# Optimization experiments

Hardware: AMD Instinct MI355X
Metric: run time of the kernel (lower is better)

## Reference

```python
import jax, jax.numpy as jnp
import numpy as np

N_NODES = 40000
N_EDGES = 640000
D = 128
BN_EPS = 1e-5
GATE_EPS = 1e-6


def _linear_params(key, d_in, d_out):
    kw, kb = jax.random.split(key)
    bound = 1.0 / np.sqrt(d_in)
    W = jax.random.uniform(kw, (d_out, d_in), jnp.float32, -bound, bound)
    b = jax.random.uniform(kb, (d_out,), jnp.float32, -bound, bound)
    return W, b


def setup_inputs() -> dict:
    key = jax.random.key(0)
    ks = jax.random.split(key, 8)
    x = jax.random.normal(ks[0], (N_NODES, D), jnp.float32)
    edge_index = jax.random.randint(ks[1], (2, N_EDGES), 0, N_NODES, jnp.int64)
    edge_attr = jax.random.normal(ks[2], (N_EDGES, D), jnp.float32)
    W_src_gate, b_src_gate = _linear_params(ks[3], D, D)
    W_dst_gate, b_dst_gate = _linear_params(ks[4], D, D)
    W_edge_gate, b_edge_gate = _linear_params(ks[5], D, D)
    W_src_update, b_src_update = _linear_params(ks[6], D, D)
    W_dst_update, b_dst_update = _linear_params(ks[7], D, D)
    return dict(
        x=x, edge_index=edge_index, edge_attr=edge_attr,
        W_src_gate=W_src_gate, b_src_gate=b_src_gate,
        W_dst_gate=W_dst_gate, b_dst_gate=b_dst_gate,
        W_edge_gate=W_edge_gate, b_edge_gate=b_edge_gate,
        W_src_update=W_src_update, b_src_update=b_src_update,
        W_dst_update=W_dst_update, b_dst_update=b_dst_update,
        bn_nodes_gamma=jnp.ones((D,), jnp.float32), bn_nodes_beta=jnp.zeros((D,), jnp.float32),
        bn_edges_gamma=jnp.ones((D,), jnp.float32), bn_edges_beta=jnp.zeros((D,), jnp.float32),
    )


def _batch_norm(z, gamma, beta):
    # training-mode BN: batch mean, biased variance (torch semantics)
    mean = jnp.mean(z, axis=0)
    var = jnp.mean(jnp.square(z - mean), axis=0)
    return gamma * (z - mean) * jax.lax.rsqrt(var + BN_EPS) + beta


def reference(x, edge_index, edge_attr,
              W_src_gate, b_src_gate, W_dst_gate, b_dst_gate,
              W_edge_gate, b_edge_gate, W_src_update, b_src_update,
              W_dst_update, b_dst_update,
              bn_nodes_gamma, bn_nodes_beta, bn_edges_gamma, bn_edges_beta):
    row, col = edge_index[0], edge_index[1]
    num_nodes = x.shape[0]
    x_row = x[row]                      # [E, D] gather
    x_col = x[col]                      # [E, D] gather
    e_src = x_row @ W_src_gate.T + b_src_gate
    e_dst = x_col @ W_dst_gate.T + b_dst_gate
    m = e_src + e_dst + edge_attr @ W_edge_gate.T + b_edge_gate  # [E, D]
    sigma = jax.nn.sigmoid(m)
    h_weighted = (x_col @ W_dst_update.T + b_dst_update) * sigma
    h_sum = jax.ops.segment_sum(h_weighted, col, num_segments=num_nodes)
    sigma_sum = jax.ops.segment_sum(sigma, col, num_segments=num_nodes)
    h_normalized = h_sum / (sigma_sum + GATE_EPS)
    x_new = x @ W_src_update.T + b_src_update + h_normalized
    x_new = jax.nn.softplus(_batch_norm(x_new, bn_nodes_gamma, bn_nodes_beta))
    y_new = jax.nn.softplus(_batch_norm(m, bn_edges_gamma, bn_edges_beta))
    x_new = x + x_new          # residual
    y_new = edge_attr + y_new  # residual
    return (x_new, y_new)
```

## Files before the change

kernel.cpp:

```cpp
#include <hip/hip_runtime.h>

#define NN 40000
#define NE 640000

typedef unsigned short u16;
typedef unsigned int u32;
typedef __attribute__((ext_vector_type(4))) float f32x4;
typedef __attribute__((ext_vector_type(8))) __bf16 bf16x8;

#define LSTR 132
#define TPW 8

__device__ __forceinline__ float bf2f(u16 u) { return __uint_as_float(((u32)u) << 16); }
__device__ __forceinline__ u16 f2bf(float f) {
  u32 u = __float_as_uint(f);
  u32 r = 0x7fffu + ((u >> 16) & 1u);
  return (u16)((u + r) >> 16);
}
__device__ __forceinline__ float splus(float v) {
  return fmaxf(v, 0.0f) + __logf(1.0f + __expf(-fabsf(v)));
}

__global__ void sniff_k(const u32* __restrict__ gamma, const u32* __restrict__ eidx,
                        u32* __restrict__ flags) {
  if (threadIdx.x == 0) {
    flags[0] = (gamma[0] == 0x3F803F80u) ? 1u : 0u;
    u32 odd = eidx[1] | eidx[3] | eidx[5] | eidx[7] |
              eidx[9] | eidx[11] | eidx[13] | eidx[15];
    flags[1] = (odd == 0u) ? 1u : 0u;
  }
}

__device__ __forceinline__ int load_col(const void* eidx, int e, u32 i64) {
  int nc = i64 ? (int)((const u32*)eidx)[2 * ((size_t)NE + e)]
               : ((const int*)eidx)[NE + e];
  return min(max(nc, 0), NN - 1);
}
__device__ __forceinline__ int load_row(const void* eidx, int e, u32 i64) {
  int nr = i64 ? (int)((const u32*)eidx)[2 * (size_t)e]
               : ((const int*)eidx)[e];
  return min(max(nr, 0), NN - 1);
}

__global__ __launch_bounds__(256) void wconv5_k(
    const float* __restrict__ W0, const float* __restrict__ W1,
    const float* __restrict__ W2, const float* __restrict__ W3,
    const float* __restrict__ W4, u16* __restrict__ out) {
  int i = blockIdx.x * 256 + threadIdx.x;
  int mtx = blockIdx.y;
  const float* W = (mtx == 0) ? W0 : (mtx == 1) ? W1 : (mtx == 2) ? W2
                 : (mtx == 3) ? W3 : W4;
  out[mtx * 16384 + i] = f2bf(W[i]);
}

__device__ __forceinline__ bf16x8 a_frag(const float* __restrict__ row, int kbase) {
  float4 f0 = *(const float4*)(row + kbase);
  float4 f1 = *(const float4*)(row + kbase + 4);
  bf16x8 a;
  a[0] = (__bf16)f0.x; a[1] = (__bf16)f0.y; a[2] = (__bf16)f0.z; a[3] = (__bf16)f0.w;
  a[4] = (__bf16)f1.x; a[5] = (__bf16)f1.y; a[6] = (__bf16)f1.z; a[7] = (__bf16)f1.w;
  return a;
}

__device__ __forceinline__ bf16x8 cvt8(float4 a, float4 b) {
  bf16x8 r;
  r[0] = (__bf16)a.x; r[1] = (__bf16)a.y; r[2] = (__bf16)a.z; r[3] = (__bf16)a.w;
  r[4] = (__bf16)b.x; r[5] = (__bf16)b.y; r[6] = (__bf16)b.z; r[7] = (__bf16)b.w;
  return r;
}

__device__ __forceinline__ void gemm16(const bf16x8 af[4], const u16* __restrict__ Wb,
                                       const float* __restrict__ bias, int lane,
                                       f32x4 acc[8]) {
  int l15 = lane & 15, lk = lane >> 4;
#pragma unroll
  for (int n = 0; n < 8; ++n) {
    float bv = bias[n * 16 + l15];
    acc[n] = (f32x4){bv, bv, bv, bv};
  }
#pragma unroll
  for (int n = 0; n < 8; ++n) {
    const u16* bp = Wb + (size_t)(n * 16 + l15) * 128 + lk * 8;
#pragma unroll
    for (int k = 0; k < 4; ++k) {
      bf16x8 b = *(const bf16x8*)(bp + 32 * k);
      acc[n] = __builtin_amdgcn_mfma_f32_16x16x32_bf16(af[k], b, acc[n], 0, 0, 0);
    }
  }
}

__device__ __forceinline__ void store_tile(u16* __restrict__ out, int m0, int lane,
                                           const f32x4 acc[8]) {
  int l15 = lane & 15, lk = lane >> 4;
#pragma unroll
  for (int n = 0; n < 8; ++n)
#pragma unroll
    for (int r = 0; r < 4; ++r)
      out[(size_t)(m0 + lk * 4 + r) * 128 + n * 16 + l15] = f2bf(acc[n][r]);
}

__global__ __launch_bounds__(256) void node_gemm_k(
    const float* __restrict__ x, const u16* __restrict__ Wb,
    const float* __restrict__ B0, const float* __restrict__ B1,
    const float* __restrict__ B2, const float* __restrict__ B3,
    u16* __restrict__ o0, u16* __restrict__ o1,
    u16* __restrict__ o2, u16* __restrict__ o3) {
  int tid = threadIdx.x, lane = tid & 63, w = tid >> 6;
  int m0 = blockIdx.x * 64 + w * 16;
  int l15 = lane & 15, lk = lane >> 4;
  const float* arow = x + (size_t)(m0 + l15) * 128;
  bf16x8 af[4];
#pragma unroll
  for (int k = 0; k < 4; ++k) af[k] = a_frag(arow, 32 * k + 8 * lk);
  f32x4 acc[8];
  gemm16(af, Wb + 0 * 16384, B0, lane, acc); store_tile(o0, m0, lane, acc);
  gemm16(af, Wb + 1 * 16384, B1, lane, acc); store_tile(o1, m0, lane, acc);
  gemm16(af, Wb + 2 * 16384, B2, lane, acc); store_tile(o2, m0, lane, acc);
  gemm16(af, Wb + 3 * 16384, B3, lane, acc); store_tile(o3, m0, lane, acc);
}

__global__ __launch_bounds__(256, 2) void edge_gemm_k(
    const float* __restrict__ ea, const u16* __restrict__ Wgb,
    const float* __restrict__ Bg, u16* __restrict__ mge) {
  __shared__ u16 mt[4][16][LSTR];
  int tid = threadIdx.x, lane = tid & 63, w = tid >> 6;
  int l15 = lane & 15, lk = lane >> 4;

  bf16x8 bf[8][4];
#pragma unroll
  for (int n = 0; n < 8; ++n)
#pragma unroll
    for (int k = 0; k < 4; ++k)
      bf[n][k] = *(const bf16x8*)(Wgb + (size_t)(n * 16 + l15) * 128 + lk * 8 + 32 * k);
  float bias[8];
#pragma unroll
  for (int n = 0; n < 8; ++n) bias[n] = Bg[n * 16 + l15];

  int base = (blockIdx.x * 4 + w) * (TPW * 16);
  const float* aptr = ea + (size_t)(base + l15) * 128 + 8 * lk;

  float4 tmp[8];
#pragma unroll
  for (int k = 0; k < 4; ++k) {
    tmp[2 * k]     = *(const float4*)(aptr + 32 * k);
    tmp[2 * k + 1] = *(const float4*)(aptr + 32 * k + 4);
  }
  bf16x8 af[4];
#pragma unroll
  for (int k = 0; k < 4; ++k) af[k] = cvt8(tmp[2 * k], tmp[2 * k + 1]);

  for (int t = 0; t < TPW; ++t) {
    if (t + 1 < TPW) {
      const float* anx = aptr + (size_t)(t + 1) * 16 * 128;
#pragma unroll
      for (int k = 0; k < 4; ++k) {
        tmp[2 * k]     = *(const float4*)(anx + 32 * k);
        tmp[2 * k + 1] = *(const float4*)(anx + 32 * k + 4);
      }
    }
    f32x4 acc[8];
#pragma unroll
    for (int n = 0; n < 8; ++n)
      acc[n] = (f32x4){bias[n], bias[n], bias[n], bias[n]};
#pragma unroll
    for (int n = 0; n < 8; ++n)
#pragma unroll
      for (int k = 0; k < 4; ++k)
        acc[n] = __builtin_amdgcn_mfma_f32_16x16x32_bf16(af[k], bf[n][k], acc[n], 0, 0, 0);
    if (t + 1 < TPW) {
#pragma unroll
      for (int k = 0; k < 4; ++k) af[k] = cvt8(tmp[2 * k], tmp[2 * k + 1]);
    }
    int e0 = base + t * 16;
#pragma unroll
    for (int n = 0; n < 8; ++n)
#pragma unroll
      for (int r = 0; r < 4; ++r)
        mt[w][lk * 4 + r][n * 16 + l15] = f2bf(acc[n][r]);
#pragma unroll
    for (int it = 0; it < 4; ++it) {
      int row = lane >> 2, ch = (lane & 3) + 4 * it;
      uint4 v = *(const uint4*)&mt[w][row][ch * 8];
      *(uint4*)(mge + (size_t)(e0 + row) * 128 + ch * 8) = v;
    }
  }
}

__global__ __launch_bounds__(256) void hist_k(const void* __restrict__ eidx,
                                              u32* __restrict__ cnt,
                                              const u32* __restrict__ flags) {
  int e = blockIdx.x * 256 + threadIdx.x;
  atomicAdd(&cnt[load_col(eidx, e, flags[1])], 1u);
}

__global__ __launch_bounds__(1024) void scan_k(const u32* __restrict__ cnt,
                                               u32* __restrict__ off,
                                               u32* __restrict__ woff) {
  __shared__ u32 wsum[16];
  __shared__ u32 carry_s;
  int tid = threadIdx.x, lane = tid & 63, wv = tid >> 6;
  if (tid == 0) carry_s = 0;
  __syncthreads();
  for (int base = 0; base < NN; base += 1024) {
    int i = base + tid;
    u32 v = (i < NN) ? cnt[i] : 0u;
    u32 s = v;
#pragma unroll
    for (int d = 1; d < 64; d <<= 1) {
      u32 t = __shfl_up(s, d);
      if (lane >= d) s += t;
    }
    if (lane == 63) wsum[wv] = s;
    __syncthreads();
    if (wv == 0 && lane < 16) {
      u32 ws = wsum[lane];
#pragma unroll
      for (int d = 1; d < 16; d <<= 1) {
        u32 t = __shfl_up(ws, d);
        if (lane >= d) ws += t;
      }
      wsum[lane] = ws;
    }
    __syncthreads();
    u32 carry = carry_s;
    u32 wpre = (wv == 0) ? 0u : wsum[wv - 1];
    u32 excl = carry + wpre + s - v;
    if (i < NN) { off[i] = excl; woff[i] = excl; }
    u32 tot = wsum[15];
    __syncthreads();
    if (tid == 0) carry_s = carry + tot;
    __syncthreads();
  }
  if (tid == 0) off[NN] = carry_s;
}

__global__ __launch_bounds__(256) void scatter2_k(const void* __restrict__ eidx,
                                                  u32* __restrict__ woff,
                                                  uint2* __restrict__ eids2,
                                                  const u32* __restrict__ flags) {
  int e = blockIdx.x * 256 + threadIdx.x;
  u32 i64 = flags[1];
  int nc = load_col(eidx, e, i64);
  int nr = load_row(eidx, e, i64);
  u32 pos = atomicAdd(&woff[nc], 1u);
  eids2[pos] = make_uint2((u32)e, (u32)nr);
}

#define NPW 4
__global__ __launch_bounds__(256) void node_gather_k(
    const u32* __restrict__ mge32, const uint2* __restrict__ eids2,
    const u32* __restrict__ off,
    const u32* __restrict__ gs32, const u32* __restrict__ gd32,
    const u32* __restrict__ us32, const u32* __restrict__ ud32,
    float* __restrict__ z, float* __restrict__ statsg) {
  __shared__ float red[512];
  int tid = threadIdx.x, lane = tid & 63, wv = tid >> 6;
  for (int i = tid; i < 512; i += 256) red[i] = 0.f;
  __syncthreads();
  float e1a = 0.f, e2a = 0.f, e1b = 0.f, e2b = 0.f;
  float t1a = 0.f, t2a = 0.f, t1b = 0.f, t2b = 0.f;
  int nbase = (blockIdx.x * 4 + wv) * NPW;
#pragma unroll
  for (int q = 0; q < NPW; ++q) {
    int n = nbase + q;
    u32 o0 = off[n], o1 = off[n + 1];
    u32 gd = gd32[(size_t)n * 64 + lane];
    float gdlo = bf2f((u16)gd), gdhi = bf2f((u16)(gd >> 16));
    float a0 = 0.f, a1 = 0.f;
    u32 p = o0;
    for (; p + 4 <= o1; p += 4) {
      uint2 er0 = eids2[p], er1 = eids2[p + 1], er2 = eids2[p + 2], er3 = eids2[p + 3];
      u32 mv0 = mge32[(size_t)er0.x * 64 + lane];
      u32 mv1 = mge32[(size_t)er1.x * 64 + lane];
      u32 mv2 = mge32[(size_t)er2.x * 64 + lane];
      u32 mv3 = mge32[(size_t)er3.x * 64 + lane];
      u32 gg0 = gs32[(size_t)er0.y * 64 + lane];
      u32 gg1 = gs32[(size_t)er1.y * 64 + lane];
      u32 gg2 = gs32[(size_t)er2.y * 64 + lane];
      u32 gg3 = gs32[(size_t)er3.y * 64 + lane];
#pragma unroll
      for (int u = 0; u < 4; ++u) {
        u32 mv = (u == 0) ? mv0 : (u == 1) ? mv1 : (u == 2) ? mv2 : mv3;
        u32 gg = (u == 0) ? gg0 : (u == 1) ? gg1 : (u == 2) ? gg2 : gg3;
        float lo = bf2f((u16)mv) + bf2f((u16)gg) + gdlo;
        float hi = bf2f((u16)(mv >> 16)) + bf2f((u16)(gg >> 16)) + gdhi;
        a0 += 1.0f / (1.0f + __expf(-lo));
        a1 += 1.0f / (1.0f + __expf(-hi));
        e1a += lo; e2a = fmaf(lo, lo, e2a);
        e1b += hi; e2b = fmaf(hi, hi, e2b);
      }
    }
    for (; p < o1; ++p) {
      uint2 er = eids2[p];
      u32 mv = mge32[(size_t)er.x * 64 + lane];
      u32 gg = gs32[(size_t)er.y * 64 + lane];
      float lo = bf2f((u16)mv) + bf2f((u16)gg) + gdlo;
      float hi = bf2f((u16)(mv >> 16)) + bf2f((u16)(gg >> 16)) + gdhi;
      a0 += 1.0f / (1.0f + __expf(-lo));
      a1 += 1.0f / (1.0f + __expf(-hi));
      e1a += lo; e2a = fmaf(lo, lo, e2a);
      e1b += hi; e2b = fmaf(hi, hi, e2b);
    }
    u32 us = us32[(size_t)n * 64 + lane];
    u32 ud = ud32[(size_t)n * 64 + lane];
    float z0 = bf2f((u16)us) + bf2f((u16)ud) * a0 / (a0 + 1e-6f);
    float z1 = bf2f((u16)(us >> 16)) + bf2f((u16)(ud >> 16)) * a1 / (a1 + 1e-6f);
    *(float2*)(z + (size_t)n * 128 + 2 * lane) = make_float2(z0, z1);
    t1a += z0; t2a = fmaf(z0, z0, t2a);
    t1b += z1; t2b = fmaf(z1, z1, t2b);
  }
  atomicAdd(&red[2 * lane], e1a);       atomicAdd(&red[2 * lane + 1], e1b);
  atomicAdd(&red[128 + 2 * lane], e2a); atomicAdd(&red[128 + 2 * lane + 1], e2b);
  atomicAdd(&red[256 + 2 * lane], t1a); atomicAdd(&red[256 + 2 * lane + 1], t1b);
  atomicAdd(&red[384 + 2 * lane], t2a); atomicAdd(&red[384 + 2 * lane + 1], t2b);
  __syncthreads();
  for (int i = tid; i < 512; i += 256) atomicAdd(&statsg[i], red[i]);
}

__global__ void stats_fin_k(const float* __restrict__ es1, const float* __restrict__ es2,
                            const float* __restrict__ ns1, const float* __restrict__ ns2,
                            const float* __restrict__ eg_, const float* __restrict__ eb_,
                            const float* __restrict__ ng_, const float* __restrict__ nb_,
                            float* __restrict__ params) {
  int d = threadIdx.x;
  float em = es1[d] * (1.0f / NE);
  float ev = fmaxf(es2[d] * (1.0f / NE) - em * em, 0.0f);
  float esc = eg_[d] * rsqrtf(ev + 1e-5f);
  params[d] = esc;
  params[128 + d] = eb_[d] - em * esc;
  float nm = ns1[d] * (1.0f / NN);
  float nv = fmaxf(ns2[d] * (1.0f / NN) - nm * nm, 0.0f);
  float nsc = ng_[d] * rsqrtf(nv + 1e-5f);
  params[256 + d] = nsc;
  params[384 + d] = nb_[d] - nm * nsc;
}

__global__ __launch_bounds__(256) void node_fin2_k(
    const float* __restrict__ x, const float* __restrict__ z,
    const float* __restrict__ params, float* __restrict__ out) {
  size_t t = (size_t)blockIdx.x * 256 + threadIdx.x;
  size_t base = t * 8;
  float4 xa = *(const float4*)(x + base);
  float4 xb = *(const float4*)(x + base + 4);
  float xv[8] = {xa.x, xa.y, xa.z, xa.w, xb.x, xb.y, xb.z, xb.w};
  float4 z0 = *(const float4*)(z + base);
  float4 z1 = *(const float4*)(z + base + 4);
  float zz[8] = {z0.x, z0.y, z0.z, z0.w, z1.x, z1.y, z1.z, z1.w};
  int d0 = (int)(base & 127);
  float o[8];
#pragma unroll
  for (int j = 0; j < 8; ++j) {
    float bnv = zz[j] * params[256 + d0 + j] + params[384 + d0 + j];
    o[j] = xv[j] + splus(bnv);
  }
  *(float4*)(out + base) = make_float4(o[0], o[1], o[2], o[3]);
  *(float4*)(out + base + 4) = make_float4(o[4], o[5], o[6], o[7]);
}

__global__ __launch_bounds__(256) void edge_fin_k(
    const float* __restrict__ edge_attr, const u16* __restrict__ mge,
    const void* __restrict__ eidx,
    const u16* __restrict__ g_src, const u16* __restrict__ g_dst,
    const float* __restrict__ params, float* __restrict__ out,
    const u32* __restrict__ flags) {
  size_t t = (size_t)blockIdx.x * 256 + threadIdx.x;
  size_t base = t * 8;
  int e = (int)(t >> 4);
  u32 i64 = flags[1];
  int row = load_row(eidx, e, i64);
  int col = load_col(eidx, e, i64);
  int d0 = (int)(base & 127);
  float4 ea = *(const float4*)(edge_attr + base);
  float4 eb = *(const float4*)(edge_attr + base + 4);
  float ev[8] = {ea.x, ea.y, ea.z, ea.w, eb.x, eb.y, eb.z, eb.w};
  uint4 mv_ = *(const uint4*)(mge + base);
  uint4 gs_ = *(const uint4*)(g_src + (size_t)row * 128 + d0);
  uint4 gd_ = *(const uint4*)(g_dst + (size_t)col * 128 + d0);
  const u16* mp = (const u16*)&mv_;
  const u16* sp = (const u16*)&gs_;
  const u16* dp = (const u16*)&gd_;
  float o[8];
#pragma unroll
  for (int j = 0; j < 8; ++j) {
    float m = bf2f(mp[j]) + bf2f(sp[j]) + bf2f(dp[j]);
    float bnv = m * params[d0 + j] + params[128 + d0 + j];
    o[j] = ev[j] + splus(bnv);
  }
  *(float4*)(out + base) = make_float4(o[0], o[1], o[2], o[3]);
  *(float4*)(out + base + 4) = make_float4(o[4], o[5], o[6], o[7]);
}

extern "C" void kernel_launch(void* const* d_in, const int* in_sizes, int n_in,
                              void* d_out, int out_size, void* d_ws, size_t ws_size,
                              hipStream_t stream) {
  const float* x        = (const float*)d_in[0];
  const void*  eidx     = d_in[1];
  const float* edge_att = (const float*)d_in[2];
  const float* Wsg = (const float*)d_in[3];  const float* bsg = (const float*)d_in[4];
  const float* Wdg = (const float*)d_in[5];  const float* bdg = (const float*)d_in[6];
  const float* Weg = (const float*)d_in[7];  const float* beg = (const float*)d_in[8];
  const float* Wsu = (const float*)d_in[9];  const float* bsu = (const float*)d_in[10];
  const float* Wdu = (const float*)d_in[11]; const float* bdu = (const float*)d_in[12];
  const float* bng = (const float*)d_in[13]; const float* bnb = (const float*)d_in[14];
  const float* beg_g = (const float*)d_in[15]; const float* beb = (const float*)d_in[16];

  char* ws = (char*)d_ws;
  u16*   g_src = (u16*)(ws + 0);
  u16*   g_dst = (u16*)(ws + 10240000);
  u16*   u_dst = (u16*)(ws + 20480000);
  u16*   u_src = (u16*)(ws + 30720000);
  float* z     = (float*)(ws + 40960000);
  float* stats = (float*)(ws + 61440000);
  u32*   flags = (u32*)(ws + 61444096);
  u16*   wbuf  = (u16*)(ws + 61448192);
  u32*   cnt   = (u32*)(ws + 61612032);
  u32*   off   = (u32*)(ws + 61772032);
  u32*   woff  = (u32*)(ws + 61932064);
  uint2* eids2 = (uint2*)(ws + 62092064);
  u16*   mge   = (u16*)(ws + 67212064);

  hipMemsetAsync(stats, 0, 4096, stream);
  hipMemsetAsync(cnt, 0, 160000, stream);

  sniff_k<<<1, 64, 0, stream>>>((const u32*)bng, (const u32*)eidx, flags);
  wconv5_k<<<dim3(64, 5), 256, 0, stream>>>(Wsg, Wdg, Wdu, Wsu, Weg, wbuf);
  node_gemm_k<<<NN / 64, 256, 0, stream>>>(x, wbuf, bsg, bdg, bdu, bsu,
                                           g_src, g_dst, u_dst, u_src);
  hist_k<<<NE / 256, 256, 0, stream>>>(eidx, cnt, flags);
  scan_k<<<1, 1024, 0, stream>>>(cnt, off, woff);
  scatter2_k<<<NE / 256, 256, 0, stream>>>(eidx, woff, eids2, flags);
  edge_gemm_k<<<NE / (64 * TPW), 256, 0, stream>>>(edge_att, wbuf + 4 * 16384, beg, mge);
  node_gather_k<<<NN / 16, 256, 0, stream>>>((const u32*)mge, eids2, off,
                                             (const u32*)g_src, (const u32*)g_dst,
                                             (const u32*)u_src, (const u32*)u_dst,
                                             z, stats);
  stats_fin_k<<<1, 128, 0, stream>>>(stats, stats + 128, stats + 256, stats + 384,
                                     beg_g, beb, bng, bnb, stats + 512);
  node_fin2_k<<<(NN * 128) / 2048, 256, 0, stream>>>(x, z, stats + 512, (float*)d_out);
  edge_fin_k<<<(NE * 128) / 2048, 256, 0, stream>>>(edge_att, mge, eidx,
                                                    g_src, g_dst, stats + 512,
                                                    (float*)d_out + (size_t)NN * 128,
                                                    flags);
}
```

Measured before the change: 586.3 us.

## Fuse gate gathers and sigmoid scatter-add into edge GEMM, drop CSR sort

```diff
diff --git a/kernel.cpp b/kernel.cpp
--- a/kernel.cpp
+++ b/kernel.cpp
@@ -10,6 +10,7 @@
 
 #define LSTR 132
 #define TPW 8
+#define NPW 4
 
 __device__ __forceinline__ float bf2f(u16 u) { return __uint_as_float(((u32)u) << 16); }
 __device__ __forceinline__ u16 f2bf(float f) {
@@ -121,10 +122,17 @@
 
 __global__ __launch_bounds__(256, 2) void edge_gemm_k(
     const float* __restrict__ ea, const u16* __restrict__ Wgb,
-    const float* __restrict__ Bg, u16* __restrict__ mge) {
-  __shared__ u16 mt[4][16][LSTR];
+    const float* __restrict__ Bg,
+    const u16* __restrict__ g_src, const u16* __restrict__ g_dst,
+    const void* __restrict__ eidx,
+    u16* __restrict__ mge, float* __restrict__ sigsum,
+    float* __restrict__ statsg, const u32* __restrict__ flags) {
+  __shared__ __align__(16) u16 mt[4][16][LSTR];
+  __shared__ __align__(16) float gt[4][16][LSTR];
+  __shared__ u32 cl[4][16];
   int tid = threadIdx.x, lane = tid & 63, w = tid >> 6;
   int l15 = lane & 15, lk = lane >> 4;
+  u32 i64 = flags[1];
 
   bf16x8 bf[8][4];
 #pragma unroll
@@ -136,6 +144,9 @@
 #pragma unroll
   for (int n = 0; n < 8; ++n) bias[n] = Bg[n * 16 + l15];
 
+  float e1[8] = {0.f, 0.f, 0.f, 0.f, 0.f, 0.f, 0.f, 0.f};
+  float e2[8] = {0.f, 0.f, 0.f, 0.f, 0.f, 0.f, 0.f, 0.f};
+
   int base = (blockIdx.x * 4 + w) * (TPW * 16);
   const float* aptr = ea + (size_t)(base + l15) * 128 + 8 * lk;
 
@@ -150,6 +161,30 @@
   for (int k = 0; k < 4; ++k) af[k] = cvt8(tmp[2 * k], tmp[2 * k + 1]);
 
   for (int t = 0; t < TPW; ++t) {
+    int e0 = base + t * 16;
+    int eg = e0 + (lane >> 2);
+    int grow = load_row(eidx, eg, i64);
+    int gcol = load_col(eidx, eg, i64);
+    if ((lane & 3) == 0) cl[w][lane >> 2] = (u32)gcol;
+#pragma unroll
+    for (int it = 0; it < 4; ++it) {
+      int ch = (lane & 3) + 4 * it;
+      uint4 gsv = *(const uint4*)(g_src + (size_t)grow * 128 + ch * 8);
+      uint4 gdv = *(const uint4*)(g_dst + (size_t)gcol * 128 + ch * 8);
+      const u16* sp = (const u16*)&gsv;
+      const u16* dp = (const u16*)&gdv;
+      float4 lo, hi;
+      lo.x = bf2f(sp[0]) + bf2f(dp[0]);
+      lo.y = bf2f(sp[1]) + bf2f(dp[1]);
+      lo.z = bf2f(sp[2]) + bf2f(dp[2]);
+      lo.w = bf2f(sp[3]) + bf2f(dp[3]);
+      hi.x = bf2f(sp[4]) + bf2f(dp[4]);
+      hi.y = bf2f(sp[5]) + bf2f(dp[5]);
+      hi.z = bf2f(sp[6]) + bf2f(dp[6]);
+      hi.w = bf2f(sp[7]) + bf2f(dp[7]);
+      *(float4*)&gt[w][lane >> 2][ch * 8]     = lo;
+      *(float4*)&gt[w][lane >> 2][ch * 8 + 4] = hi;
+    }
     if (t + 1 < TPW) {
       const float* anx = aptr + (size_t)(t + 1) * 16 * 128;
 #pragma unroll
@@ -167,16 +202,25 @@
 #pragma unroll
       for (int k = 0; k < 4; ++k)
         acc[n] = __builtin_amdgcn_mfma_f32_16x16x32_bf16(af[k], bf[n][k], acc[n], 0, 0, 0);
+    u32 cr[4];
+#pragma unroll
+    for (int r = 0; r < 4; ++r) cr[r] = cl[w][lk * 4 + r];
+#pragma unroll
+    for (int n = 0; n < 8; ++n) {
+#pragma unroll
+      for (int r = 0; r < 4; ++r) {
+        float mv = acc[n][r] + gt[w][lk * 4 + r][n * 16 + l15];
+        float sg = 1.0f / (1.0f + __expf(-mv));
+        atomicAdd(&sigsum[(size_t)cr[r] * 128 + n * 16 + l15], sg);
+        e1[n] += mv;
+        e2[n] = fmaf(mv, mv, e2[n]);
+        mt[w][lk * 4 + r][n * 16 + l15] = f2bf(mv);
+      }
+    }
     if (t + 1 < TPW) {
 #pragma unroll
       for (int k = 0; k < 4; ++k) af[k] = cvt8(tmp[2 * k], tmp[2 * k + 1]);
     }
-    int e0 = base + t * 16;
-#pragma unroll
-    for (int n = 0; n < 8; ++n)
-#pragma unroll
-      for (int r = 0; r < 4; ++r)
-        mt[w][lk * 4 + r][n * 16 + l15] = f2bf(acc[n][r]);
 #pragma unroll
     for (int it = 0; it < 4; ++it) {
       int row = lane >> 2, ch = (lane & 3) + 4 * it;
@@ -184,137 +228,42 @@
       *(uint4*)(mge + (size_t)(e0 + row) * 128 + ch * 8) = v;
     }
   }
-}
-
-__global__ __launch_bounds__(256) void hist_k(const void* __restrict__ eidx,
-                                              u32* __restrict__ cnt,
-                                              const u32* __restrict__ flags) {
-  int e = blockIdx.x * 256 + threadIdx.x;
-  atomicAdd(&cnt[load_col(eidx, e, flags[1])], 1u);
-}
-
-__global__ __launch_bounds__(1024) void scan_k(const u32* __restrict__ cnt,
-                                               u32* __restrict__ off,
-                                               u32* __restrict__ woff) {
-  __shared__ u32 wsum[16];
-  __shared__ u32 carry_s;
+#pragma unroll
+  for (int n = 0; n < 8; ++n) {
+    float s1 = e1[n], s2 = e2[n];
+    s1 += __shfl_xor(s1, 16); s1 += __shfl_xor(s1, 32);
+    s2 += __shfl_xor(s2, 16); s2 += __shfl_xor(s2, 32);
+    if (lk == 0) {
+      atomicAdd(&statsg[n * 16 + l15], s1);
+      atomicAdd(&statsg[128 + n * 16 + l15], s2);
+    }
+  }
+}
+
+__global__ __launch_bounds__(256) void node_stats_k(
+    const float* __restrict__ sigsum, const u32* __restrict__ us32,
+    const u32* __restrict__ ud32, float* __restrict__ statsg) {
+  __shared__ float red[256];
   int tid = threadIdx.x, lane = tid & 63, wv = tid >> 6;
-  if (tid == 0) carry_s = 0;
+  for (int i = tid; i < 256; i += 256) red[i] = 0.f;
   __syncthreads();
-  for (int base = 0; base < NN; base += 1024) {
-    int i = base + tid;
-    u32 v = (i < NN) ? cnt[i] : 0u;
-    u32 s = v;
-#pragma unroll
-    for (int d = 1; d < 64; d <<= 1) {
-      u32 t = __shfl_up(s, d);
-      if (lane >= d) s += t;
-    }
-    if (lane == 63) wsum[wv] = s;
-    __syncthreads();
-    if (wv == 0 && lane < 16) {
-      u32 ws = wsum[lane];
-#pragma unroll
-      for (int d = 1; d < 16; d <<= 1) {
-        u32 t = __shfl_up(ws, d);
-        if (lane >= d) ws += t;
-      }
-      wsum[lane] = ws;
-    }
-    __syncthreads();
-    u32 carry = carry_s;
-    u32 wpre = (wv == 0) ? 0u : wsum[wv - 1];
-    u32 excl = carry + wpre + s - v;
-    if (i < NN) { off[i] = excl; woff[i] = excl; }
-    u32 tot = wsum[15];
-    __syncthreads();
-    if (tid == 0) carry_s = carry + tot;
-    __syncthreads();
-  }
-  if (tid == 0) off[NN] = carry_s;
-}
-
-__global__ __launch_bounds__(256) void scatter2_k(const void* __restrict__ eidx,
-                                                  u32* __restrict__ woff,
-                                                  uint2* __restrict__ eids2,
-                                                  const u32* __restrict__ flags) {
-  int e = blockIdx.x * 256 + threadIdx.x;
-  u32 i64 = flags[1];
-  int nc = load_col(eidx, e, i64);
-  int nr = load_row(eidx, e, i64);
-  u32 pos = atomicAdd(&woff[nc], 1u);
-  eids2[pos] = make_uint2((u32)e, (u32)nr);
-}
-
-#define NPW 4
-__global__ __launch_bounds__(256) void node_gather_k(
-    const u32* __restrict__ mge32, const uint2* __restrict__ eids2,
-    const u32* __restrict__ off,
-    const u32* __restrict__ gs32, const u32* __restrict__ gd32,
-    const u32* __restrict__ us32, const u32* __restrict__ ud32,
-    float* __restrict__ z, float* __restrict__ statsg) {
-  __shared__ float red[512];
-  int tid = threadIdx.x, lane = tid & 63, wv = tid >> 6;
-  for (int i = tid; i < 512; i += 256) red[i] = 0.f;
-  __syncthreads();
-  float e1a = 0.f, e2a = 0.f, e1b = 0.f, e2b = 0.f;
   float t1a = 0.f, t2a = 0.f, t1b = 0.f, t2b = 0.f;
   int nbase = (blockIdx.x * 4 + wv) * NPW;
 #pragma unroll
   for (int q = 0; q < NPW; ++q) {
     int n = nbase + q;
-    u32 o0 = off[n], o1 = off[n + 1];
-    u32 gd = gd32[(size_t)n * 64 + lane];
-    float gdlo = bf2f((u16)gd), gdhi = bf2f((u16)(gd >> 16));
-    float a0 = 0.f, a1 = 0.f;
-    u32 p = o0;
-    for (; p + 4 <= o1; p += 4) {
-      uint2 er0 = eids2[p], er1 = eids2[p + 1], er2 = eids2[p + 2], er3 = eids2[p + 3];
-      u32 mv0 = mge32[(size_t)er0.x * 64 + lane];
-      u32 mv1 = mge32[(size_t)er1.x * 64 + lane];
-      u32 mv2 = mge32[(size_t)er2.x * 64 + lane];
-      u32 mv3 = mge32[(size_t)er3.x * 64 + lane];
-      u32 gg0 = gs32[(size_t)er0.y * 64 + lane];
-      u32 gg1 = gs32[(size_t)er1.y * 64 + lane];
-      u32 gg2 = gs32[(size_t)er2.y * 64 + lane];
-      u32 gg3 = gs32[(size_t)er3.y * 64 + lane];
-#pragma unroll
-      for (int u = 0; u < 4; ++u) {
-        u32 mv = (u == 0) ? mv0 : (u == 1) ? mv1 : (u == 2) ? mv2 : mv3;
-        u32 gg = (u == 0) ? gg0 : (u == 1) ? gg1 : (u == 2) ? gg2 : gg3;
-        float lo = bf2f((u16)mv) + bf2f((u16)gg) + gdlo;
-        float hi = bf2f((u16)(mv >> 16)) + bf2f((u16)(gg >> 16)) + gdhi;
-        a0 += 1.0f / (1.0f + __expf(-lo));
-        a1 += 1.0f / (1.0f + __expf(-hi));
-        e1a += lo; e2a = fmaf(lo, lo, e2a);
-        e1b += hi; e2b = fmaf(hi, hi, e2b);
-      }
-    }
-    for (; p < o1; ++p) {
-      uint2 er = eids2[p];
-      u32 mv = mge32[(size_t)er.x * 64 + lane];
-      u32 gg = gs32[(size_t)er.y * 64 + lane];
-      float lo = bf2f((u16)mv) + bf2f((u16)gg) + gdlo;
-      float hi = bf2f((u16)(mv >> 16)) + bf2f((u16)(gg >> 16)) + gdhi;
-      a0 += 1.0f / (1.0f + __expf(-lo));
-      a1 += 1.0f / (1.0f + __expf(-hi));
-      e1a += lo; e2a = fmaf(lo, lo, e2a);
-      e1b += hi; e2b = fmaf(hi, hi, e2b);
-    }
+    float2 a2 = *(const float2*)(sigsum + (size_t)n * 128 + 2 * lane);
     u32 us = us32[(size_t)n * 64 + lane];
     u32 ud = ud32[(size_t)n * 64 + lane];
-    float z0 = bf2f((u16)us) + bf2f((u16)ud) * a0 / (a0 + 1e-6f);
-    float z1 = bf2f((u16)(us >> 16)) + bf2f((u16)(ud >> 16)) * a1 / (a1 + 1e-6f);
-    *(float2*)(z + (size_t)n * 128 + 2 * lane) = make_float2(z0, z1);
+    float z0 = bf2f((u16)us) + bf2f((u16)ud) * a2.x / (a2.x + 1e-6f);
+    float z1 = bf2f((u16)(us >> 16)) + bf2f((u16)(ud >> 16)) * a2.y / (a2.y + 1e-6f);
     t1a += z0; t2a = fmaf(z0, z0, t2a);
     t1b += z1; t2b = fmaf(z1, z1, t2b);
   }
-  atomicAdd(&red[2 * lane], e1a);       atomicAdd(&red[2 * lane + 1], e1b);
-  atomicAdd(&red[128 + 2 * lane], e2a); atomicAdd(&red[128 + 2 * lane + 1], e2b);
-  atomicAdd(&red[256 + 2 * lane], t1a); atomicAdd(&red[256 + 2 * lane + 1], t1b);
-  atomicAdd(&red[384 + 2 * lane], t2a); atomicAdd(&red[384 + 2 * lane + 1], t2b);
+  atomicAdd(&red[2 * lane], t1a);       atomicAdd(&red[2 * lane + 1], t1b);
+  atomicAdd(&red[128 + 2 * lane], t2a); atomicAdd(&red[128 + 2 * lane + 1], t2b);
   __syncthreads();
-  for (int i = tid; i < 512; i += 256) atomicAdd(&statsg[i], red[i]);
+  for (int i = tid; i < 256; i += 256) atomicAdd(&statsg[256 + i], red[i]);
 }
 
 __global__ void stats_fin_k(const float* __restrict__ es1, const float* __restrict__ es2,
@@ -336,21 +285,28 @@
 }
 
 __global__ __launch_bounds__(256) void node_fin2_k(
-    const float* __restrict__ x, const float* __restrict__ z,
+    const float* __restrict__ x, const float* __restrict__ sigsum,
+    const u16* __restrict__ us, const u16* __restrict__ ud,
     const float* __restrict__ params, float* __restrict__ out) {
   size_t t = (size_t)blockIdx.x * 256 + threadIdx.x;
   size_t base = t * 8;
+  int d0 = (int)(base & 127);
   float4 xa = *(const float4*)(x + base);
   float4 xb = *(const float4*)(x + base + 4);
   float xv[8] = {xa.x, xa.y, xa.z, xa.w, xb.x, xb.y, xb.z, xb.w};
-  float4 z0 = *(const float4*)(z + base);
-  float4 z1 = *(const float4*)(z + base + 4);
-  float zz[8] = {z0.x, z0.y, z0.z, z0.w, z1.x, z1.y, z1.z, z1.w};
-  int d0 = (int)(base & 127);
+  float4 s0 = *(const float4*)(sigsum + base);
+  float4 s1 = *(const float4*)(sigsum + base + 4);
+  float av[8] = {s0.x, s0.y, s0.z, s0.w, s1.x, s1.y, s1.z, s1.w};
+  uint4 usv = *(const uint4*)(us + base);
+  uint4 udv = *(const uint4*)(ud + base);
+  const u16* up = (const u16*)&usv;
+  const u16* dp = (const u16*)&udv;
   float o[8];
 #pragma unroll
   for (int j = 0; j < 8; ++j) {
-    float bnv = zz[j] * params[256 + d0 + j] + params[384 + d0 + j];
+    float a = av[j];
+    float z = bf2f(up[j]) + bf2f(dp[j]) * a / (a + 1e-6f);
+    float bnv = z * params[256 + d0 + j] + params[384 + d0 + j];
     o[j] = xv[j] + splus(bnv);
   }
   *(float4*)(out + base) = make_float4(o[0], o[1], o[2], o[3]);
@@ -359,30 +315,19 @@
 
 __global__ __launch_bounds__(256) void edge_fin_k(
     const float* __restrict__ edge_attr, const u16* __restrict__ mge,
-    const void* __restrict__ eidx,
-    const u16* __restrict__ g_src, const u16* __restrict__ g_dst,
-    const float* __restrict__ params, float* __restrict__ out,
-    const u32* __restrict__ flags) {
+    const float* __restrict__ params, float* __restrict__ out) {
   size_t t = (size_t)blockIdx.x * 256 + threadIdx.x;
   size_t base = t * 8;
-  int e = (int)(t >> 4);
-  u32 i64 = flags[1];
-  int row = load_row(eidx, e, i64);
-  int col = load_col(eidx, e, i64);
   int d0 = (int)(base & 127);
   float4 ea = *(const float4*)(edge_attr + base);
   float4 eb = *(const float4*)(edge_attr + base + 4);
   float ev[8] = {ea.x, ea.y, ea.z, ea.w, eb.x, eb.y, eb.z, eb.w};
   uint4 mv_ = *(const uint4*)(mge + base);
-  uint4 gs_ = *(const uint4*)(g_src + (size_t)row * 128 + d0);
-  uint4 gd_ = *(const uint4*)(g_dst + (size_t)col * 128 + d0);
   const u16* mp = (const u16*)&mv_;
-  const u16* sp = (const u16*)&gs_;
-  const u16* dp = (const u16*)&gd_;
   float o[8];
 #pragma unroll
   for (int j = 0; j < 8; ++j) {
-    float m = bf2f(mp[j]) + bf2f(sp[j]) + bf2f(dp[j]);
+    float m = bf2f(mp[j]);
     float bnv = m * params[d0 + j] + params[128 + d0 + j];
     o[j] = ev[j] + splus(bnv);
   }
@@ -405,40 +350,32 @@
   const float* beg_g = (const float*)d_in[15]; const float* beb = (const float*)d_in[16];
 
   char* ws = (char*)d_ws;
-  u16*   g_src = (u16*)(ws + 0);
-  u16*   g_dst = (u16*)(ws + 10240000);
-  u16*   u_dst = (u16*)(ws + 20480000);
-  u16*   u_src = (u16*)(ws + 30720000);
-  float* z     = (float*)(ws + 40960000);
-  float* stats = (float*)(ws + 61440000);
-  u32*   flags = (u32*)(ws + 61444096);
-  u16*   wbuf  = (u16*)(ws + 61448192);
-  u32*   cnt   = (u32*)(ws + 61612032);
-  u32*   off   = (u32*)(ws + 61772032);
-  u32*   woff  = (u32*)(ws + 61932064);
-  uint2* eids2 = (uint2*)(ws + 62092064);
-  u16*   mge   = (u16*)(ws + 67212064);
+  u16*   g_src  = (u16*)(ws + 0);
+  u16*   g_dst  = (u16*)(ws + 10240000);
+  u16*   u_dst  = (u16*)(ws + 20480000);
+  u16*   u_src  = (u16*)(ws + 30720000);
+  float* sigsum = (float*)(ws + 40960000);
+  float* stats  = (float*)(ws + 61440000);
+  u32*   flags  = (u32*)(ws + 61444096);
+  u16*   wbuf   = (u16*)(ws + 61448192);
+  u16*   mge    = (u16*)(ws + 61612032);
 
   hipMemsetAsync(stats, 0, 4096, stream);
-  hipMemsetAsync(cnt, 0, 160000, stream);
+  hipMemsetAsync(sigsum, 0, 20480000, stream);
 
   sniff_k<<<1, 64, 0, stream>>>((const u32*)bng, (const u32*)eidx, flags);
   wconv5_k<<<dim3(64, 5), 256, 0, stream>>>(Wsg, Wdg, Wdu, Wsu, Weg, wbuf);
   node_gemm_k<<<NN / 64, 256, 0, stream>>>(x, wbuf, bsg, bdg, bdu, bsu,
                                            g_src, g_dst, u_dst, u_src);
-  hist_k<<<NE / 256, 256, 0, stream>>>(eidx, cnt, flags);
-  scan_k<<<1, 1024, 0, stream>>>(cnt, off, woff);
-  scatter2_k<<<NE / 256, 256, 0, stream>>>(eidx, woff, eids2, flags);
-  edge_gemm_k<<<NE / (64 * TPW), 256, 0, stream>>>(edge_att, wbuf + 4 * 16384, beg, mge);
-  node_gather_k<<<NN / 16, 256, 0, stream>>>((const u32*)mge, eids2, off,
-                                             (const u32*)g_src, (const u32*)g_dst,
-                                             (const u32*)u_src, (const u32*)u_dst,
-                                             z, stats);
+  edge_gemm_k<<<NE / (64 * TPW), 256, 0, stream>>>(edge_att, wbuf + 4 * 16384, beg,
+                                                   g_src, g_dst, eidx,
+                                                   mge, sigsum, stats, flags);
+  node_stats_k<<<NN / 16, 256, 0, stream>>>(sigsum, (const u32*)u_src,
+                                            (const u32*)u_dst, stats);
   stats_fin_k<<<1, 128, 0, stream>>>(stats, stats + 128, stats + 256, stats + 384,
                                      beg_g, beb, bng, bnb, stats + 512);
-  node_fin2_k<<<(NN * 128) / 2048, 256, 0, stream>>>(x, z, stats + 512, (float*)d_out);
-  edge_fin_k<<<(NE * 128) / 2048, 256, 0, stream>>>(edge_att, mge, eidx,
-                                                    g_src, g_dst, stats + 512,
-                                                    (float*)d_out + (size_t)NN * 128,
-                                                    flags);
-}
+  node_fin2_k<<<(NN * 128) / 2048, 256, 0, stream>>>(x, sigsum, u_src, u_dst,
+                                                     stats + 512, (float*)d_out);
+  edge_fin_k<<<(NE * 128) / 2048, 256, 0, stream>>>(edge_att, mge, stats + 512,
+                                                    (float*)d_out + (size_t)NN * 128);
+}
```

Measured after the change: 748.8 us. +27.7%, slower.
